# Performance work log

Measured on AMD Instinct MI355X. Metric: run time of the kernel, lower is better.

Reference implementation:

```python
import jax, jax.numpy as jnp
import numpy as np

NUM_CLUSTERS = 64
DIM = 128
ALPHA = 100.0


def setup_inputs() -> dict:
    key = jax.random.key(0)
    k1, k2 = jax.random.split(key)
    x = jax.random.normal(k1, (32, 4096, DIM), dtype=jnp.float32)
    centroids = jax.random.uniform(k2, (NUM_CLUSTERS, DIM), dtype=jnp.float32)
    return {"x": x, "centroids": centroids}


def reference(x, centroids):
    # x: [B, N, D], centroids: [K, D]
    # Euclidean distances (torch.cdist p=2): [B, N, K]
    x2 = jnp.sum(x * x, axis=-1, keepdims=True)            # [B, N, 1]
    c2 = jnp.sum(centroids * centroids, axis=-1)            # [K]
    xc = jnp.einsum('bnd,kd->bnk', x, centroids)            # [B, N, K]
    dist2 = jnp.maximum(x2 + c2[None, None, :] - 2.0 * xc, 0.0)
    distances = jnp.sqrt(dist2)
    soft_assign = jax.nn.softmax(-ALPHA * distances, axis=2)  # [B, N, K]
    # vlad[b,k,:] = sum_n a[b,n,k] * (x[b,n,:] - c[k,:])
    vlad = jnp.einsum('bnk,bnd->bkd', soft_assign, x) \
         - jnp.sum(soft_assign, axis=1)[:, :, None] * centroids[None, :, :]
    B = x.shape[0]
    vlad = vlad.reshape(B, -1)
    # F.normalize(p=2, dim=1) with default eps=1e-12
    norm = jnp.maximum(jnp.linalg.norm(vlad, axis=1, keepdims=True), 1e-12)
    return vlad / norm
```

## Files before the change

### kernel.cpp

```cpp
#include <hip/hip_runtime.h>

typedef _Float16 half8 __attribute__((ext_vector_type(8)));
typedef float floatx4 __attribute__((ext_vector_type(4)));

static constexpr int NB  = 32;
static constexpr int NP  = 4096;
static constexpr int DD  = 128;
static constexpr int KC  = 64;
static constexpr int TN  = 64;
static constexpr int TPB = 4;
static constexpr int SLOTS = NP / (TPB * TN);
static constexpr int STP = 72;

#define ALPHA_  100.0f
#define LOG2E_  1.44269504088896f

#define LGKM_BARRIER() asm volatile("s_waitcnt lgkmcnt(0)\ns_barrier" ::: "memory")

__global__ __launch_bounds__(256, 2)
void vlad_main(const float* __restrict__ xg, const float* __restrict__ cg,
               float* __restrict__ vp, float* __restrict__ cpart)
{
    __shared__ __align__(16) _Float16 sxt[2][DD][STP];
    __shared__ __align__(16) _Float16 sat[2][KC][STP];
    __shared__ float sc2[KC];

    const int tid  = threadIdx.x;
    const int lane = tid & 63;
    const int w    = tid >> 6;
    const int l15  = lane & 15;
    const int quad = lane >> 4;
    const int b    = blockIdx.y;
    const int s    = blockIdx.x;
    const float* xb = xg + (size_t)b * NP * DD;

    const int nloc = w*16 + l15;
    const int scol = nloc ^ (quad << 4);
    const float* xpt = xb + (size_t)(s*TPB*TN + nloc)*DD + quad*8;

    float4 fa[4], fb[4];
#pragma unroll
    for (int ks = 0; ks < 4; ++ks) {
        fa[ks] = *(const float4*)(xpt + ks*32);
        fb[ks] = *(const float4*)(xpt + ks*32 + 4);
    }

    half8 chi[4][4];
    float c2p[4];
#pragma unroll
    for (int mt = 0; mt < 4; ++mt) {
        c2p[mt] = 0.f;
#pragma unroll
        for (int ks = 0; ks < 4; ++ks) {
            const float* p = cg + (mt*16 + l15)*DD + ks*32 + quad*8;
            float4 a  = *(const float4*)p;
            float4 bb = *(const float4*)(p + 4);
            half8 h;
            h[0]=(_Float16)a.x;  h[1]=(_Float16)a.y;  h[2]=(_Float16)a.z;  h[3]=(_Float16)a.w;
            h[4]=(_Float16)bb.x; h[5]=(_Float16)bb.y; h[6]=(_Float16)bb.z; h[7]=(_Float16)bb.w;
            chi[mt][ks] = h;
            c2p[mt] += a.x*a.x + a.y*a.y + a.z*a.z + a.w*a.w
                     + bb.x*bb.x + bb.y*bb.y + bb.z*bb.z + bb.w*bb.w;
        }
    }
#pragma unroll
    for (int mt = 0; mt < 4; ++mt) {
        float s2 = c2p[mt];
        s2 += __shfl_xor(s2, 16);
        s2 += __shfl_xor(s2, 32);
        if (quad == 0 && w == 0) sc2[mt*16 + l15] = s2;
    }
    LGKM_BARRIER();

    floatx4 acc2[8];
#pragma unroll
    for (int i = 0; i < 8; ++i) acc2[i] = (floatx4){0.f, 0.f, 0.f, 0.f};
    floatx4 accs = (floatx4){0.f, 0.f, 0.f, 0.f};

    half8 onesf;
#pragma unroll
    for (int j = 0; j < 8; ++j) onesf[j] = (_Float16)((l15 == 0) ? 1.0f : 0.0f);

#pragma unroll
    for (int tt = 0; tt < TPB; ++tt) {
        const int pb = tt & 1;

        half8 xf[4];
        float ssq = 0.f;
#pragma unroll
        for (int ks = 0; ks < 4; ++ks) {
            half8 h;
            h[0]=(_Float16)fa[ks].x; h[1]=(_Float16)fa[ks].y;
            h[2]=(_Float16)fa[ks].z; h[3]=(_Float16)fa[ks].w;
            h[4]=(_Float16)fb[ks].x; h[5]=(_Float16)fb[ks].y;
            h[6]=(_Float16)fb[ks].z; h[7]=(_Float16)fb[ks].w;
            xf[ks] = h;
            ssq += fa[ks].x*fa[ks].x + fa[ks].y*fa[ks].y + fa[ks].z*fa[ks].z + fa[ks].w*fa[ks].w
                 + fb[ks].x*fb[ks].x + fb[ks].y*fb[ks].y + fb[ks].z*fb[ks].z + fb[ks].w*fb[ks].w;
        }

        if (tt + 1 < TPB) {
            const float* xr = xpt + (size_t)(tt + 1) * TN * DD;
#pragma unroll
            for (int ks = 0; ks < 4; ++ks) {
                fa[ks] = *(const float4*)(xr + ks*32);
                fb[ks] = *(const float4*)(xr + ks*32 + 4);
            }
        }

#pragma unroll
        for (int ks = 0; ks < 4; ++ks)
#pragma unroll
            for (int j = 0; j < 8; ++j)
                sxt[pb][ks*32 + quad*8 + j][scol] = xf[ks][j];

        floatx4 acc1[4];
#pragma unroll
        for (int mt = 0; mt < 4; ++mt) acc1[mt] = (floatx4){0.f, 0.f, 0.f, 0.f};
#pragma unroll
        for (int ks = 0; ks < 4; ++ks)
#pragma unroll
            for (int mt = 0; mt < 4; ++mt)
                acc1[mt] = __builtin_amdgcn_mfma_f32_16x16x32_f16(chi[mt][ks], xf[ks], acc1[mt], 0, 0, 0);
        ssq += __shfl_xor(ssq, 16);
        ssq += __shfl_xor(ssq, 32);

        float dist[4][4];
#pragma unroll
        for (int mt = 0; mt < 4; ++mt) {
            floatx4 c2v = *(const floatx4*)&sc2[mt*16 + quad*4];
#pragma unroll
            for (int r = 0; r < 4; ++r) {
                float d2 = ssq + c2v[r] - 2.f*acc1[mt][r];
                dist[mt][r] = sqrtf(fmaxf(d2, 0.f));
            }
        }
        float dmin = dist[0][0];
#pragma unroll
        for (int mt = 0; mt < 4; ++mt)
#pragma unroll
            for (int r = 0; r < 4; ++r) dmin = fminf(dmin, dist[mt][r]);
        dmin = fminf(dmin, __shfl_xor(dmin, 16));
        dmin = fminf(dmin, __shfl_xor(dmin, 32));
        float pv[4][4];
        float psum = 0.f;
#pragma unroll
        for (int mt = 0; mt < 4; ++mt)
#pragma unroll
            for (int r = 0; r < 4; ++r) {
                float e = exp2f((dmin - dist[mt][r]) * (ALPHA_ * LOG2E_));
                pv[mt][r] = e; psum += e;
            }
        psum += __shfl_xor(psum, 16);
        psum += __shfl_xor(psum, 32);
        float invs = 1.0f / psum;
#pragma unroll
        for (int mt = 0; mt < 4; ++mt)
#pragma unroll
            for (int r = 0; r < 4; ++r)
                sat[pb][mt*16 + quad*4 + r][scol] = (_Float16)(pv[mt][r] * invs);

        LGKM_BARRIER();

#pragma unroll
        for (int ks2 = 0; ks2 < 2; ++ks2) {
            const int nbase = ks2*32 + quad*8;
            half8 af = *(const half8*)&sat[pb][w*16 + l15][nbase ^ ((l15 >> 2) << 4)];
            accs = __builtin_amdgcn_mfma_f32_16x16x32_f16(af, onesf, accs, 0, 0, 0);
#pragma unroll
            for (int nt = 0; nt < 8; ++nt) {
                const int d = nt*16 + l15;
                half8 bf = *(const half8*)&sxt[pb][d][nbase ^ (((d >> 3) & 3) << 4)];
                acc2[nt] = __builtin_amdgcn_mfma_f32_16x16x32_f16(af, bf, acc2[nt], 0, 0, 0);
            }
        }
    }

    float* slot = vp + ((size_t)b*SLOTS + s) * (KC*DD);
#pragma unroll
    for (int nt = 0; nt < 8; ++nt)
#pragma unroll
        for (int r = 0; r < 4; ++r) {
            int k = w*16 + quad*4 + r;
            int d = nt*16 + l15;
            slot[k*DD + d] = acc2[nt][r];
        }
    if (l15 == 0) {
#pragma unroll
        for (int r = 0; r < 4; ++r)
            cpart[((size_t)b*SLOTS + s)*KC + w*16 + quad*4 + r] = accs[r];
    }
}

__global__ __launch_bounds__(256)
void vlad_reduce(const float* __restrict__ vp, const float* __restrict__ cpart,
                 const float* __restrict__ cg, float* __restrict__ vfull,
                 float* __restrict__ ssp)
{
    __shared__ float scs[KC];
    __shared__ float red[4];
    const int b   = blockIdx.x >> 3;
    const int q   = blockIdx.x & 7;
    const int tid = threadIdx.x;

    if (tid < KC) {
        float cs = 0.f;
#pragma unroll
        for (int si = 0; si < SLOTS; ++si)
            cs += cpart[((size_t)b*SLOTS + si)*KC + tid];
        scs[tid] = cs;
    }
    __syncthreads();

    const int idx = q*1024 + tid*4;
    const float* vpb = vp + (size_t)b*SLOTS*(KC*DD) + idx;
    float4 a = {0.f, 0.f, 0.f, 0.f};
#pragma unroll
    for (int si = 0; si < SLOTS; ++si) {
        float4 t = *(const float4*)(vpb + (size_t)si*(KC*DD));
        a.x += t.x; a.y += t.y; a.z += t.z; a.w += t.w;
    }
    float cs = scs[idx >> 7];
    float4 cv = *(const float4*)(cg + idx);
    a.x -= cs*cv.x; a.y -= cs*cv.y; a.z -= cs*cv.z; a.w -= cs*cv.w;
    *(float4*)(vfull + (size_t)b*(KC*DD) + idx) = a;
    float ss = a.x*a.x + a.y*a.y + a.z*a.z + a.w*a.w;
#pragma unroll
    for (int m = 1; m < 64; m <<= 1) ss += __shfl_xor(ss, m);
    if ((tid & 63) == 0) red[tid >> 6] = ss;
    __syncthreads();
    if (tid == 0) ssp[b*8 + q] = red[0] + red[1] + red[2] + red[3];
}

__global__ __launch_bounds__(256)
void vlad_norm(const float* __restrict__ vfull, const float* __restrict__ ssp,
               float* __restrict__ out)
{
    const int b   = blockIdx.x;
    const int tid = threadIdx.x;
    float tot = 0.f;
#pragma unroll
    for (int q = 0; q < 8; ++q) tot += ssp[b*8 + q];
    float scale = 1.0f / fmaxf(sqrtf(tot), 1e-12f);
#pragma unroll
    for (int i = 0; i < 8; ++i) {
        int idx = i*1024 + tid*4;
        float4 v = *(const float4*)(vfull + (size_t)b*(KC*DD) + idx);
        v.x *= scale; v.y *= scale; v.z *= scale; v.w *= scale;
        *(float4*)(out + (size_t)b*(KC*DD) + idx) = v;
    }
}

extern "C" void kernel_launch(void* const* d_in, const int* in_sizes, int n_in,
                              void* d_out, int out_size, void* d_ws, size_t ws_size,
                              hipStream_t stream)
{
    (void)in_sizes; (void)n_in; (void)out_size; (void)ws_size;
    const float* x = (const float*)d_in[0];
    const float* c = (const float*)d_in[1];
    float* out   = (float*)d_out;
    float* vp    = (float*)d_ws;
    float* cpart = vp + (size_t)NB*SLOTS*KC*DD;
    float* vfull = cpart + (size_t)NB*SLOTS*KC;
    float* ssp   = vfull + (size_t)NB*KC*DD;

    vlad_main<<<dim3(SLOTS, NB), 256, 0, stream>>>(x, c, vp, cpart);
    vlad_reduce<<<NB*8, 256, 0, stream>>>(vp, cpart, c, vfull, ssp);
    vlad_norm<<<NB, 256, 0, stream>>>(vfull, ssp, out);
}
```

Baseline: 113.7 us.

## Accumulate VLAD partials with atomics and fuse reduce and normalize kernels

The main kernel now accumulates its per-slot partial sums directly into a zeroed full VLAD buffer with float atomicAdd, replacing per-slot partial writes. The reduce and normalize kernels merge into a single per-batch finalize kernel that keeps values in registers. This removes the partial-sum round trip through memory and one kernel launch, at the cost of a memset, atomic contention across 16 slots per batch, a finalize grid of only 32 blocks, and non-deterministic summation order.

```diff
diff --git a/kernel.cpp b/kernel.cpp
--- a/kernel.cpp
+++ b/kernel.cpp
@@ -19,7 +19,7 @@
 
 __global__ __launch_bounds__(256, 2)
 void vlad_main(const float* __restrict__ xg, const float* __restrict__ cg,
-               float* __restrict__ vp, float* __restrict__ cpart)
+               float* __restrict__ vfull, float* __restrict__ csum)
 {
     __shared__ __align__(16) _Float16 sxt[2][DD][STP];
     __shared__ __align__(16) _Float16 sat[2][KC][STP];
@@ -176,78 +176,59 @@
         }
     }
 
-    float* slot = vp + ((size_t)b*SLOTS + s) * (KC*DD);
+    float* vb = vfull + (size_t)b * (KC*DD);
 #pragma unroll
     for (int nt = 0; nt < 8; ++nt)
 #pragma unroll
         for (int r = 0; r < 4; ++r) {
             int k = w*16 + quad*4 + r;
             int d = nt*16 + l15;
-            slot[k*DD + d] = acc2[nt][r];
+            atomicAdd(&vb[k*DD + d], acc2[nt][r]);
         }
     if (l15 == 0) {
 #pragma unroll
         for (int r = 0; r < 4; ++r)
-            cpart[((size_t)b*SLOTS + s)*KC + w*16 + quad*4 + r] = accs[r];
+            atomicAdd(&csum[(size_t)b*KC + w*16 + quad*4 + r], accs[r]);
     }
 }
 
 __global__ __launch_bounds__(256)
-void vlad_reduce(const float* __restrict__ vp, const float* __restrict__ cpart,
-                 const float* __restrict__ cg, float* __restrict__ vfull,
-                 float* __restrict__ ssp)
+void vlad_finalize(const float* __restrict__ vfull, const float* __restrict__ csum,
+                   const float* __restrict__ cg, float* __restrict__ out)
 {
     __shared__ float scs[KC];
     __shared__ float red[4];
-    const int b   = blockIdx.x >> 3;
-    const int q   = blockIdx.x & 7;
+    const int b   = blockIdx.x;
     const int tid = threadIdx.x;
 
-    if (tid < KC) {
-        float cs = 0.f;
-#pragma unroll
-        for (int si = 0; si < SLOTS; ++si)
-            cs += cpart[((size_t)b*SLOTS + si)*KC + tid];
-        scs[tid] = cs;
-    }
+    if (tid < KC) scs[tid] = csum[(size_t)b*KC + tid];
     __syncthreads();
 
-    const int idx = q*1024 + tid*4;
-    const float* vpb = vp + (size_t)b*SLOTS*(KC*DD) + idx;
-    float4 a = {0.f, 0.f, 0.f, 0.f};
-#pragma unroll
-    for (int si = 0; si < SLOTS; ++si) {
-        float4 t = *(const float4*)(vpb + (size_t)si*(KC*DD));
-        a.x += t.x; a.y += t.y; a.z += t.z; a.w += t.w;
-    }
-    float cs = scs[idx >> 7];
-    float4 cv = *(const float4*)(cg + idx);
-    a.x -= cs*cv.x; a.y -= cs*cv.y; a.z -= cs*cv.z; a.w -= cs*cv.w;
-    *(float4*)(vfull + (size_t)b*(KC*DD) + idx) = a;
-    float ss = a.x*a.x + a.y*a.y + a.z*a.z + a.w*a.w;
+    const float* vb = vfull + (size_t)b*(KC*DD);
+    float4 v[8];
+    float ss = 0.f;
+#pragma unroll
+    for (int i = 0; i < 8; ++i) {
+        const int idx = i*1024 + tid*4;
+        float4 a  = *(const float4*)(vb + idx);
+        float4 cv = *(const float4*)(cg + idx);
+        float cs  = scs[idx >> 7];
+        a.x -= cs*cv.x; a.y -= cs*cv.y; a.z -= cs*cv.z; a.w -= cs*cv.w;
+        v[i] = a;
+        ss += a.x*a.x + a.y*a.y + a.z*a.z + a.w*a.w;
+    }
 #pragma unroll
     for (int m = 1; m < 64; m <<= 1) ss += __shfl_xor(ss, m);
     if ((tid & 63) == 0) red[tid >> 6] = ss;
     __syncthreads();
-    if (tid == 0) ssp[b*8 + q] = red[0] + red[1] + red[2] + red[3];
-}
-
-__global__ __launch_bounds__(256)
-void vlad_norm(const float* __restrict__ vfull, const float* __restrict__ ssp,
-               float* __restrict__ out)
-{
-    const int b   = blockIdx.x;
-    const int tid = threadIdx.x;
-    float tot = 0.f;
-#pragma unroll
-    for (int q = 0; q < 8; ++q) tot += ssp[b*8 + q];
+    float tot = red[0] + red[1] + red[2] + red[3];
     float scale = 1.0f / fmaxf(sqrtf(tot), 1e-12f);
 #pragma unroll
     for (int i = 0; i < 8; ++i) {
-        int idx = i*1024 + tid*4;
-        float4 v = *(const float4*)(vfull + (size_t)b*(KC*DD) + idx);
-        v.x *= scale; v.y *= scale; v.z *= scale; v.w *= scale;
-        *(float4*)(out + (size_t)b*(KC*DD) + idx) = v;
+        const int idx = i*1024 + tid*4;
+        float4 a = v[i];
+        a.x *= scale; a.y *= scale; a.z *= scale; a.w *= scale;
+        *(float4*)(out + (size_t)b*(KC*DD) + idx) = a;
     }
 }
 
@@ -259,12 +240,11 @@
     const float* x = (const float*)d_in[0];
     const float* c = (const float*)d_in[1];
     float* out   = (float*)d_out;
-    float* vp    = (float*)d_ws;
-    float* cpart = vp + (size_t)NB*SLOTS*KC*DD;
-    float* vfull = cpart + (size_t)NB*SLOTS*KC;
-    float* ssp   = vfull + (size_t)NB*KC*DD;
-
-    vlad_main<<<dim3(SLOTS, NB), 256, 0, stream>>>(x, c, vp, cpart);
-    vlad_reduce<<<NB*8, 256, 0, stream>>>(vp, cpart, c, vfull, ssp);
-    vlad_norm<<<NB, 256, 0, stream>>>(vfull, ssp, out);
+    float* vfull = (float*)d_ws;
+    float* csum  = vfull + (size_t)NB*KC*DD;
+
+    hipMemsetAsync(d_ws, 0, ((size_t)NB*KC*DD + (size_t)NB*KC)*sizeof(float), stream);
+
+    vlad_main<<<dim3(SLOTS, NB), 256, 0, stream>>>(x, c, vfull, csum);
+    vlad_finalize<<<NB, 256, 0, stream>>>(vfull, csum, c, out);
 }
```

Result: slower. 118.3 us (+4.1%).
